# Kernel optimization log

Measured on AMD Instinct MI355X. Metric: run time of the kernel, lower is better.

## Reference

```python
import jax, jax.numpy as jnp
import numpy as np

N = 100000   # nodes
DEG = 4      # fixed out-degree (>2 so every node survives the c>2 mask)
E = N * DEG  # edges
IN = 128
H = 256


def _lin_params(key, fan_out, fan_in, bias=True):
    k1, k2 = jax.random.split(key)
    W = 0.05 * jax.random.normal(k1, (fan_out, fan_in), jnp.float32)
    if bias:
        b = 0.05 * jax.random.normal(k2, (fan_out,), jnp.float32)
        return W, b
    return W


def setup_inputs() -> dict:
    key = jax.random.key(0)
    ks = jax.random.split(key, 12)
    x = jax.random.normal(ks[0], (N, IN), jnp.float32)
    # every node has exactly DEG outgoing edges -> out-degree 4 > 2 for all nodes
    src = jnp.repeat(jnp.arange(N, dtype=jnp.int32), DEG)
    dst = jax.random.randint(ks[1], (E,), 0, N, dtype=jnp.int32)
    edge_index = jnp.stack([src, dst])  # [2, E]
    batch = jnp.zeros((N,), jnp.int32)
    Wr0, br0 = _lin_params(ks[2], H, IN)
    Ws0 = _lin_params(ks[3], H, IN, bias=False)
    Wr1, br1 = _lin_params(ks[4], H, H)
    Ws1 = _lin_params(ks[5], H, H, bias=False)
    Wr2, br2 = _lin_params(ks[6], H, H)
    Ws2 = _lin_params(ks[7], H, H, bias=False)
    Wsp1, bsp1 = _lin_params(ks[8], 1, H)
    Wsp2, bsp2 = _lin_params(ks[9], 1, H)
    Wl, bl = _lin_params(ks[10], 1, 2)
    return dict(x=x, edge_index=edge_index, batch=batch,
                Wr0=Wr0, br0=br0, Ws0=Ws0,
                Wr1=Wr1, br1=br1, Ws1=Ws1,
                Wr2=Wr2, br2=br2, Ws2=Ws2,
                Wsp1=Wsp1, bsp1=bsp1, Wsp2=Wsp2, bsp2=bsp2,
                Wl=Wl, bl=bl)


def reference(x, edge_index, batch, Wr0, br0, Ws0, Wr1, br1, Ws1,
              Wr2, br2, Ws2, Wsp1, bsp1, Wsp2, bsp2, Wl, bl):
    src, dst = edge_index[0], edge_index[1]

    def gconv(h, Wr, br, Ws):
        # PyG GraphConv(aggr='add'): out_i = W_rel @ sum_{j->i} h_j + b + W_root @ h_i
        agg = jax.ops.segment_sum(h[src], dst, num_segments=N)
        return jax.nn.relu(agg @ Wr.T + br + h @ Ws.T)

    h = gconv(x, Wr0, br0, Ws0)
    h = gconv(h, Wr1, br1, Ws1)
    h = gconv(h, Wr2, br2, Ws2)

    # unique(edge_index[0], counts) ; keep source nodes with out-degree > 2
    deg = jax.ops.segment_sum(jnp.ones((E,), h.dtype), src, num_segments=N)
    sel = jnp.nonzero(deg > 2, size=N, fill_value=0)[0]  # all N nodes by construction
    xs = h[sel].reshape(-1, 2 * H)  # pair consecutive nodes
    x1, x2 = xs[:, :H], xs[:, H:]
    out = jnp.concatenate([jax.nn.relu(x1 @ Wsp1.T + bsp1),
                           jax.nn.relu(x2 @ Wsp2.T + bsp2)], axis=1)
    y = jax.nn.sigmoid(out @ Wl.T + bl)  # split=True branch
    return y, xs, x1, x2
```

## Files before the change

kernel.cpp:

```cpp
#include <hip/hip_runtime.h>
#include <hip/hip_bf16.h>
#include <math.h>

#define NNODES 100000
#define NEDGES 400000
#define INDIM  128
#define HDIM   256
#define MAXDEG 32

#define BM 64
#define BN 256
#define BK 64
#define MTILES 1563

typedef __attribute__((ext_vector_type(8))) short short8;
typedef __attribute__((ext_vector_type(8))) unsigned short ushort8v;
typedef __attribute__((ext_vector_type(4))) float f32x4;

__device__ __forceinline__ float bf2f(unsigned short u) {
    union { unsigned int i; float f; } v; v.i = ((unsigned int)u) << 16; return v.f;
}
__device__ __forceinline__ unsigned short f2bf(float f) {
    union { float f; unsigned int i; } v; v.f = f;
    unsigned int r = v.i + 0x7fffu + ((v.i >> 16) & 1u);
    return (unsigned short)(r >> 16);
}

__device__ __forceinline__ void async_load16(const void* g, void* l) {
    __builtin_amdgcn_global_load_lds(
        (const __attribute__((address_space(1))) unsigned int*)g,
        (__attribute__((address_space(3))) unsigned int*)l,
        16, 0, 0);
}

#define XB_BLOCKS 12500
#define W0_BLOCKS 256
#define W1_BLOCKS 512
#define EL_BLOCKS 1563
#define PREP_BLOCKS (XB_BLOCKS + W0_BLOCKS + 2 * W1_BLOCKS + EL_BLOCKS)

__global__ void prep_kernel(const float* __restrict__ x, unsigned short* __restrict__ xb,
                            const float* __restrict__ Wr0, const float* __restrict__ Ws0,
                            unsigned short* __restrict__ B0,
                            const float* __restrict__ Wr1, const float* __restrict__ Ws1,
                            unsigned short* __restrict__ B1,
                            const float* __restrict__ Wr2, const float* __restrict__ Ws2,
                            unsigned short* __restrict__ B2,
                            const int* __restrict__ ei, int* __restrict__ cnt,
                            int* __restrict__ elist) {
    int b = blockIdx.x;
    if (b < XB_BLOCKS) {
        int i = b * 256 + threadIdx.x;
        float4 v = ((const float4*)x)[i];
        ushort4 o; o.x = f2bf(v.x); o.y = f2bf(v.y); o.z = f2bf(v.z); o.w = f2bf(v.w);
        ((ushort4*)xb)[i] = o;
        return;
    }
    b -= XB_BLOCKS;
    if (b < W0_BLOCKS + 2 * W1_BLOCKS) {
        const float *Wr, *Ws; unsigned short* B; int K;
        if (b < W0_BLOCKS)               { Wr = Wr0; Ws = Ws0; B = B0; K = INDIM; }
        else if (b < W0_BLOCKS + W1_BLOCKS) { Wr = Wr1; Ws = Ws1; B = B1; K = HDIM; b -= W0_BLOCKS; }
        else                              { Wr = Wr2; Ws = Ws2; B = B2; K = HDIM; b -= W0_BLOCKS + W1_BLOCKS; }
        int idx = b * 256 + threadIdx.x;
        int n = idx / (2 * K);
        int k = idx - n * 2 * K;
        float v = (k < K) ? Wr[n * K + k] : Ws[n * K + (k - K)];
        B[idx] = f2bf(v);
        return;
    }
    b -= W0_BLOCKS + 2 * W1_BLOCKS;
    int e = b * 256 + threadIdx.x;
    if (e < NEDGES) {
        int d = ei[NEDGES + e];
        int s = ei[e];
        int pos = atomicAdd(&cnt[d], 1);
        if (pos < MAXDEG) elist[d * MAXDEG + pos] = s;
    }
}

template<int MODE>
__global__ __launch_bounds__(256)
void fused_gconv(const unsigned short* __restrict__ h,
                 const int* __restrict__ cnt, const int* __restrict__ elist,
                 int K, const unsigned short* __restrict__ B, const float* __restrict__ bias,
                 unsigned short* __restrict__ hout,
                 float* __restrict__ xs, float* __restrict__ x1o, float* __restrict__ x2o,
                 const float* __restrict__ Wsp1, const float* __restrict__ Wsp2,
                 float* __restrict__ spart) {
    __shared__ __align__(16) unsigned char smem[65536];
    unsigned short* Agg = (unsigned short*)smem;
    unsigned short* Bsh = (unsigned short*)(smem + 32768);

    const int tid  = threadIdx.x;
    const int lane = tid & 63;
    const int wv   = tid >> 6;
    const int m0   = blockIdx.x * BM;
    const int Ktot = 2 * K;

    const int lane31 = lane & 31;
    const int hw     = lane >> 5;
    int pn = m0 + wv * 16 + (lane >> 2);
    if (pn >= NNODES) pn = NNODES - 1;
    const int4 elv = ((const int4*)(elist + (size_t)pn * MAXDEG))[lane & 3];
    int cnode = m0 + wv * 16 + (lane & 15);
    if (cnode >= NNODES) cnode = NNODES - 1;
    const int cv = cnt[cnode];

    #pragma unroll
    for (int it = 0; it < 8; it++) {
        int idx = it * 256 + tid;
        int row = idx >> 3, seg = idx & 7;
        int gseg = seg ^ (row & 7);
        async_load16(B + (size_t)row * Ktot + gseg * 8, &Bsh[idx * 8]);
    }

    if (K == 256) {
        for (int rd = 0; rd < 8; rd++) {
            const int iw = rd * 2 + hw;
            int cA = __shfl(cv, rd * 2);
            int cB = __shfl(cv, rd * 2 + 1);
            if (cA > MAXDEG) cA = MAXDEG;
            if (cB > MAXDEG) cB = MAXDEG;
            const int c    = hw ? cB : cA;
            const int cmax = cA > cB ? cA : cB;
            int node = m0 + wv * 16 + iw;
            if (node >= NNODES) node = NNODES - 1;
            float a[8];
            #pragma unroll
            for (int i = 0; i < 8; i++) a[i] = 0.f;
            for (int j0 = 0; j0 < cmax; j0 += 4) {
                int4 e;
                if (j0 < 16) {
                    int src = iw * 4 + (j0 >> 2);
                    e.x = __shfl(elv.x, src); e.y = __shfl(elv.y, src);
                    e.z = __shfl(elv.z, src); e.w = __shfl(elv.w, src);
                } else {
                    e = ((const int4*)(elist + (size_t)node * MAXDEG))[j0 >> 2];
                }
                int rem = c - j0;
                ushort8v v0 = {0,0,0,0,0,0,0,0}, v1 = v0, v2 = v0, v3 = v0;
                if (rem > 0) v0 = ((const ushort8v*)(h + (size_t)e.x * 256))[lane31];
                if (rem > 1) v1 = ((const ushort8v*)(h + (size_t)e.y * 256))[lane31];
                if (rem > 2) v2 = ((const ushort8v*)(h + (size_t)e.z * 256))[lane31];
                if (rem > 3) v3 = ((const ushort8v*)(h + (size_t)e.w * 256))[lane31];
                #pragma unroll
                for (int i = 0; i < 8; i++)
                    a[i] += bf2f(v0[i]) + bf2f(v1[i]) + bf2f(v2[i]) + bf2f(v3[i]);
            }
            int r = wv * 16 + iw;
            int sgp = (lane31 & ~7) | ((lane31 ^ r) & 7);
            ushort8v o;
            #pragma unroll
            for (int i = 0; i < 8; i++) o[i] = f2bf(a[i]);
            *(ushort8v*)&Agg[r * 256 + sgp * 8] = o;
        }
    } else {
        for (int rd = 0; rd < 8; rd++) {
            const int iw = rd * 2 + hw;
            int cA = __shfl(cv, rd * 2);
            int cB = __shfl(cv, rd * 2 + 1);
            if (cA > MAXDEG) cA = MAXDEG;
            if (cB > MAXDEG) cB = MAXDEG;
            const int c    = hw ? cB : cA;
            const int cmax = cA > cB ? cA : cB;
            int node = m0 + wv * 16 + iw;
            if (node >= NNODES) node = NNODES - 1;
            float a0 = 0.f, a1 = 0.f, a2 = 0.f, a3 = 0.f;
            for (int j0 = 0; j0 < cmax; j0 += 4) {
                int4 e;
                if (j0 < 16) {
                    int src = iw * 4 + (j0 >> 2);
                    e.x = __shfl(elv.x, src); e.y = __shfl(elv.y, src);
                    e.z = __shfl(elv.z, src); e.w = __shfl(elv.w, src);
                } else {
                    e = ((const int4*)(elist + (size_t)node * MAXDEG))[j0 >> 2];
                }
                int rem = c - j0;
                ushort4 v0 = {0,0,0,0}, v1 = {0,0,0,0}, v2 = {0,0,0,0}, v3 = {0,0,0,0};
                if (rem > 0) v0 = ((const ushort4*)(h + (size_t)e.x * 128))[lane31];
                if (rem > 1) v1 = ((const ushort4*)(h + (size_t)e.y * 128))[lane31];
                if (rem > 2) v2 = ((const ushort4*)(h + (size_t)e.z * 128))[lane31];
                if (rem > 3) v3 = ((const ushort4*)(h + (size_t)e.w * 128))[lane31];
                a0 += bf2f(v0.x) + bf2f(v1.x) + bf2f(v2.x) + bf2f(v3.x);
                a1 += bf2f(v0.y) + bf2f(v1.y) + bf2f(v2.y) + bf2f(v3.y);
                a2 += bf2f(v0.z) + bf2f(v1.z) + bf2f(v2.z) + bf2f(v3.z);
                a3 += bf2f(v0.w) + bf2f(v1.w) + bf2f(v2.w) + bf2f(v3.w);
            }
            int r = wv * 16 + iw;
            int sg = lane31 >> 1;
            int sgp = (sg & ~7) | ((sg ^ r) & 7);
            ushort4 o; o.x = f2bf(a0); o.y = f2bf(a1); o.z = f2bf(a2); o.w = f2bf(a3);
            *(ushort4*)&Agg[r * 128 + sgp * 8 + (lane31 & 1) * 4] = o;
        }
    }

    f32x4 acc[4][4];
    #pragma unroll
    for (int i = 0; i < 4; i++)
        #pragma unroll
        for (int j = 0; j < 4; j++)
            acc[i][j] = (f32x4){0.f, 0.f, 0.f, 0.f};

    for (int k0 = 0; k0 < Ktot; k0 += BK) {
        if (k0 >= K) {
            #pragma unroll
            for (int it = 0; it < 2; it++) {
                int idx = it * 256 + tid;
                int row = idx >> 3, seg = idx & 7;
                int gseg = seg ^ (row & 7);
                int grow = m0 + row; if (grow >= NNODES) grow = NNODES - 1;
                async_load16(h + (size_t)grow * K + (k0 - K) + gseg * 8, &Agg[idx * 8]);
            }
        }
        if (k0 > 0) {
            #pragma unroll
            for (int it = 0; it < 8; it++) {
                int idx = it * 256 + tid;
                int row = idx >> 3, seg = idx & 7;
                int gseg = seg ^ (row & 7);
                async_load16(B + (size_t)row * Ktot + k0 + gseg * 8, &Bsh[idx * 8]);
            }
        }
        __syncthreads();

        #pragma unroll
        for (int half = 0; half < 2; half++) {
            short8 af[4], bfr[4];
            if (k0 < K) {
                #pragma unroll
                for (int mt = 0; mt < 4; mt++) {
                    int ml = mt * 16 + (lane & 15);
                    int sg = (k0 >> 3) + half * 4 + (lane >> 4);
                    int sgp = (sg & ~7) | ((sg ^ ml) & 7);
                    af[mt] = *(const short8*)&Agg[ml * K + sgp * 8];
                }
            } else {
                #pragma unroll
                for (int mt = 0; mt < 4; mt++) {
                    int ml  = mt * 16 + (lane & 15);
                    int seg = half * 4 + (lane >> 4);
                    int ps  = seg ^ (ml & 7);
                    af[mt] = *(const short8*)&Agg[ml * BK + ps * 8];
                }
            }
            #pragma unroll
            for (int nt = 0; nt < 4; nt++) {
                int nl  = wv * 64 + nt * 16 + (lane & 15);
                int seg = half * 4 + (lane >> 4);
                int ps  = seg ^ (nl & 7);
                bfr[nt] = *(const short8*)&Bsh[nl * BK + ps * 8];
            }
            #pragma unroll
            for (int mt = 0; mt < 4; mt++)
                #pragma unroll
                for (int nt = 0; nt < 4; nt++)
                    acc[mt][nt] = __builtin_amdgcn_mfma_f32_16x16x32_bf16(
                        af[mt], bfr[nt], acc[mt][nt], 0, 0, 0);
        }
        __syncthreads();
    }

    float* bounce = (float*)smem;
    float* wb = bounce + wv * (16 * 68);
    const int q    = lane & 3;
    const int rrow = lane >> 2;

    #pragma unroll
    for (int mt = 0; mt < 4; mt++) {
        __syncthreads();
        #pragma unroll
        for (int nt = 0; nt < 4; nt++)
            #pragma unroll
            for (int rr = 0; rr < 4; rr++)
                wb[((lane >> 4) * 4 + rr) * 68 + nt * 16 + (lane & 15)] = acc[mt][nt][rr];
        __syncthreads();

        int grow = m0 + mt * 16 + rrow;
        int gc   = wv * 64 + q * 16;
        float4 v[4];
        #pragma unroll
        for (int s = 0; s < 4; s++)
            v[s] = ((const float4*)(wb + rrow * 68 + q * 16))[s];

        if (grow < NNODES) {
            const float4* bv = (const float4*)(bias + gc);
            #pragma unroll
            for (int s = 0; s < 4; s++) {
                float4 b4 = bv[s];
                v[s].x = fmaxf(v[s].x + b4.x, 0.f);
                v[s].y = fmaxf(v[s].y + b4.y, 0.f);
                v[s].z = fmaxf(v[s].z + b4.z, 0.f);
                v[s].w = fmaxf(v[s].w + b4.w, 0.f);
            }
            if (MODE == 0) {
                ushort8v o0, o1;
                o0[0]=f2bf(v[0].x); o0[1]=f2bf(v[0].y); o0[2]=f2bf(v[0].z); o0[3]=f2bf(v[0].w);
                o0[4]=f2bf(v[1].x); o0[5]=f2bf(v[1].y); o0[6]=f2bf(v[1].z); o0[7]=f2bf(v[1].w);
                o1[0]=f2bf(v[2].x); o1[1]=f2bf(v[2].y); o1[2]=f2bf(v[2].z); o1[3]=f2bf(v[2].w);
                o1[4]=f2bf(v[3].x); o1[5]=f2bf(v[3].y); o1[6]=f2bf(v[3].z); o1[7]=f2bf(v[3].w);
                ushort8v* dst = (ushort8v*)(hout + (size_t)grow * HDIM + gc);
                dst[0] = o0; dst[1] = o1;
            } else {
                float4* xsp = (float4*)(xs + (size_t)grow * HDIM + gc);
                #pragma unroll
                for (int s = 0; s < 4; s++) xsp[s] = v[s];
                float* xo = (grow & 1) ? x2o : x1o;
                float4* xop = (float4*)(xo + (size_t)(grow >> 1) * HDIM + gc);
                #pragma unroll
                for (int s = 0; s < 4; s++) xop[s] = v[s];
                const float* wsp = (grow & 1) ? Wsp2 : Wsp1;
                const float4* wv4 = (const float4*)(wsp + gc);
                float p = 0.f;
                #pragma unroll
                for (int s = 0; s < 4; s++) {
                    float4 w4 = wv4[s];
                    p += v[s].x * w4.x + v[s].y * w4.y + v[s].z * w4.z + v[s].w * w4.w;
                }
                p += __shfl_xor(p, 1);
                p += __shfl_xor(p, 2);
                if (q == 0) atomicAdd(&spart[grow], p);
            }
        }
    }
}

__global__ void finalize_kernel(const float* __restrict__ spart, const float* __restrict__ bsp1,
                                const float* __restrict__ bsp2, const float* __restrict__ Wl,
                                const float* __restrict__ bl, float* __restrict__ y) {
    int p = blockIdx.x * 256 + threadIdx.x;
    if (p < NNODES / 2) {
        float s1 = spart[2 * p]     + bsp1[0]; s1 = s1 > 0.f ? s1 : 0.f;
        float s2 = spart[2 * p + 1] + bsp2[0]; s2 = s2 > 0.f ? s2 : 0.f;
        float t = s1 * Wl[0] + s2 * Wl[1] + bl[0];
        y[p] = 1.f / (1.f + expf(-t));
    }
}

extern "C" void kernel_launch(void* const* d_in, const int* in_sizes, int n_in,
                              void* d_out, int out_size, void* d_ws, size_t ws_size,
                              hipStream_t stream) {
    const float* x    = (const float*)d_in[0];
    const int*   ei   = (const int*)d_in[1];
    const float* Wr0  = (const float*)d_in[3];
    const float* br0  = (const float*)d_in[4];
    const float* Ws0  = (const float*)d_in[5];
    const float* Wr1  = (const float*)d_in[6];
    const float* br1  = (const float*)d_in[7];
    const float* Ws1  = (const float*)d_in[8];
    const float* Wr2  = (const float*)d_in[9];
    const float* br2  = (const float*)d_in[10];
    const float* Ws2  = (const float*)d_in[11];
    const float* Wsp1 = (const float*)d_in[12];
    const float* bsp1 = (const float*)d_in[13];
    const float* Wsp2 = (const float*)d_in[14];
    const float* bsp2 = (const float*)d_in[15];
    const float* Wl   = (const float*)d_in[16];
    const float* bl   = (const float*)d_in[17];

    char* ws = (char*)d_ws;
    size_t off = 0;
    auto alloc = [&](size_t bytes) -> void* {
        void* p = ws + off;
        off += (bytes + 255) & ~(size_t)255;
        return p;
    };
    int*            cnt   = (int*)alloc((size_t)NNODES * 4);
    float*          spart = (float*)alloc((size_t)NNODES * 4);
    size_t zero_bytes = off;
    int*            elist = (int*)alloc((size_t)NNODES * MAXDEG * 4);
    unsigned short* xb    = (unsigned short*)alloc((size_t)NNODES * INDIM * 2);
    unsigned short* hA    = (unsigned short*)alloc((size_t)NNODES * HDIM * 2);
    unsigned short* hB    = (unsigned short*)alloc((size_t)NNODES * HDIM * 2);
    unsigned short* B0    = (unsigned short*)alloc((size_t)HDIM * 2 * INDIM * 2);
    unsigned short* B1    = (unsigned short*)alloc((size_t)HDIM * 2 * HDIM * 2);
    unsigned short* B2    = (unsigned short*)alloc((size_t)HDIM * 2 * HDIM * 2);

    float* y  = (float*)d_out;
    float* xs = y + 50000;
    float* x1 = xs + (size_t)50000 * 512;
    float* x2 = x1 + (size_t)50000 * 256;

    hipMemsetAsync(ws, 0, zero_bytes, stream);
    prep_kernel<<<PREP_BLOCKS, 256, 0, stream>>>(x, xb, Wr0, Ws0, B0, Wr1, Ws1, B1,
                                                 Wr2, Ws2, B2, ei, cnt, elist);

    fused_gconv<0><<<MTILES, 256, 0, stream>>>(xb, cnt, elist, INDIM, B0, br0, hA,
                                               nullptr, nullptr, nullptr,
                                               nullptr, nullptr, nullptr);
    fused_gconv<0><<<MTILES, 256, 0, stream>>>(hA, cnt, elist, HDIM, B1, br1, hB,
                                               nullptr, nullptr, nullptr,
                                               nullptr, nullptr, nullptr);
    fused_gconv<1><<<MTILES, 256, 0, stream>>>(hB, cnt, elist, HDIM, B2, br2, nullptr,
                                               xs, x1, x2, Wsp1, Wsp2, spart);
    finalize_kernel<<<(NNODES / 2 + 255) / 256, 256, 0, stream>>>(
        spart, bsp1, bsp2, Wl, bl, y);
}
```

Measured before the change: 603.7 us.

## Load GEMM operands directly from global, halve LDS, template K

Drops the LDS staging of the weight matrix B and of the root-feature tile. MFMA fragments are now read straight from global memory, and the root (h @ Ws) term is computed first so it can overlap the aggregation. LDS shrinks from 64KB to 32KB, K becomes a template parameter, and launch bounds request 3 blocks per CU to raise occupancy. The cost is uncoalesced, repeated global and L2 reads of B across waves with no LDS reuse, plus higher register pressure from fully unrolled loops.

```diff
diff --git a/kernel.cpp b/kernel.cpp
--- a/kernel.cpp
+++ b/kernel.cpp
@@ -24,13 +24,6 @@
     union { float f; unsigned int i; } v; v.f = f;
     unsigned int r = v.i + 0x7fffu + ((v.i >> 16) & 1u);
     return (unsigned short)(r >> 16);
-}
-
-__device__ __forceinline__ void async_load16(const void* g, void* l) {
-    __builtin_amdgcn_global_load_lds(
-        (const __attribute__((address_space(1))) unsigned int*)g,
-        (__attribute__((address_space(3))) unsigned int*)l,
-        16, 0, 0);
 }
 
 #define XB_BLOCKS 12500
@@ -79,24 +72,23 @@
     }
 }
 
-template<int MODE>
-__global__ __launch_bounds__(256)
+template<int MODE, int K>
+__global__ __launch_bounds__(256, 3)
 void fused_gconv(const unsigned short* __restrict__ h,
                  const int* __restrict__ cnt, const int* __restrict__ elist,
-                 int K, const unsigned short* __restrict__ B, const float* __restrict__ bias,
+                 const unsigned short* __restrict__ B, const float* __restrict__ bias,
                  unsigned short* __restrict__ hout,
                  float* __restrict__ xs, float* __restrict__ x1o, float* __restrict__ x2o,
                  const float* __restrict__ Wsp1, const float* __restrict__ Wsp2,
                  float* __restrict__ spart) {
-    __shared__ __align__(16) unsigned char smem[65536];
+    __shared__ __align__(16) unsigned char smem[32768];
     unsigned short* Agg = (unsigned short*)smem;
-    unsigned short* Bsh = (unsigned short*)(smem + 32768);
 
     const int tid  = threadIdx.x;
     const int lane = tid & 63;
     const int wv   = tid >> 6;
     const int m0   = blockIdx.x * BM;
-    const int Ktot = 2 * K;
+    constexpr int Ktot = 2 * K;
 
     const int lane31 = lane & 31;
     const int hw     = lane >> 5;
@@ -107,15 +99,7 @@
     if (cnode >= NNODES) cnode = NNODES - 1;
     const int cv = cnt[cnode];
 
-    #pragma unroll
-    for (int it = 0; it < 8; it++) {
-        int idx = it * 256 + tid;
-        int row = idx >> 3, seg = idx & 7;
-        int gseg = seg ^ (row & 7);
-        async_load16(B + (size_t)row * Ktot + gseg * 8, &Bsh[idx * 8]);
-    }
-
-    if (K == 256) {
+    if constexpr (K == 256) {
         for (int rd = 0; rd < 8; rd++) {
             const int iw = rd * 2 + hw;
             int cA = __shfl(cv, rd * 2);
@@ -202,54 +186,24 @@
         for (int j = 0; j < 4; j++)
             acc[i][j] = (f32x4){0.f, 0.f, 0.f, 0.f};
 
-    for (int k0 = 0; k0 < Ktot; k0 += BK) {
-        if (k0 >= K) {
-            #pragma unroll
-            for (int it = 0; it < 2; it++) {
-                int idx = it * 256 + tid;
-                int row = idx >> 3, seg = idx & 7;
-                int gseg = seg ^ (row & 7);
-                int grow = m0 + row; if (grow >= NNODES) grow = NNODES - 1;
-                async_load16(h + (size_t)grow * K + (k0 - K) + gseg * 8, &Agg[idx * 8]);
-            }
-        }
-        if (k0 > 0) {
-            #pragma unroll
-            for (int it = 0; it < 8; it++) {
-                int idx = it * 256 + tid;
-                int row = idx >> 3, seg = idx & 7;
-                int gseg = seg ^ (row & 7);
-                async_load16(B + (size_t)row * Ktot + k0 + gseg * 8, &Bsh[idx * 8]);
-            }
-        }
-        __syncthreads();
-
+    const int l15  = lane & 15;
+    const int seg0 = lane >> 4;
+
+    #pragma unroll
+    for (int k0 = 0; k0 < K; k0 += BK) {
         #pragma unroll
         for (int half = 0; half < 2; half++) {
+            const int seg = half * 4 + seg0;
             short8 af[4], bfr[4];
-            if (k0 < K) {
-                #pragma unroll
-                for (int mt = 0; mt < 4; mt++) {
-                    int ml = mt * 16 + (lane & 15);
-                    int sg = (k0 >> 3) + half * 4 + (lane >> 4);
-                    int sgp = (sg & ~7) | ((sg ^ ml) & 7);
-                    af[mt] = *(const short8*)&Agg[ml * K + sgp * 8];
-                }
-            } else {
-                #pragma unroll
-                for (int mt = 0; mt < 4; mt++) {
-                    int ml  = mt * 16 + (lane & 15);
-                    int seg = half * 4 + (lane >> 4);
-                    int ps  = seg ^ (ml & 7);
-                    af[mt] = *(const short8*)&Agg[ml * BK + ps * 8];
-                }
+            #pragma unroll
+            for (int mt = 0; mt < 4; mt++) {
+                int grow = m0 + mt * 16 + l15; if (grow >= NNODES) grow = NNODES - 1;
+                af[mt] = *(const short8*)(h + (size_t)grow * K + k0 + seg * 8);
             }
             #pragma unroll
             for (int nt = 0; nt < 4; nt++) {
-                int nl  = wv * 64 + nt * 16 + (lane & 15);
-                int seg = half * 4 + (lane >> 4);
-                int ps  = seg ^ (nl & 7);
-                bfr[nt] = *(const short8*)&Bsh[nl * BK + ps * 8];
+                int nl = wv * 64 + nt * 16 + l15;
+                bfr[nt] = *(const short8*)(B + (size_t)nl * Ktot + K + k0 + seg * 8);
             }
             #pragma unroll
             for (int mt = 0; mt < 4; mt++)
@@ -258,7 +212,35 @@
                     acc[mt][nt] = __builtin_amdgcn_mfma_f32_16x16x32_bf16(
                         af[mt], bfr[nt], acc[mt][nt], 0, 0, 0);
         }
-        __syncthreads();
+    }
+
+    __syncthreads();
+
+    #pragma unroll
+    for (int k0 = 0; k0 < K; k0 += BK) {
+        #pragma unroll
+        for (int half = 0; half < 2; half++) {
+            const int seg = half * 4 + seg0;
+            short8 af[4], bfr[4];
+            #pragma unroll
+            for (int nt = 0; nt < 4; nt++) {
+                int nl = wv * 64 + nt * 16 + l15;
+                bfr[nt] = *(const short8*)(B + (size_t)nl * Ktot + k0 + seg * 8);
+            }
+            #pragma unroll
+            for (int mt = 0; mt < 4; mt++) {
+                int ml = mt * 16 + l15;
+                int sg = (k0 >> 3) + seg;
+                int sgp = (sg & ~7) | ((sg ^ ml) & 7);
+                af[mt] = *(const short8*)&Agg[ml * K + sgp * 8];
+            }
+            #pragma unroll
+            for (int mt = 0; mt < 4; mt++)
+                #pragma unroll
+                for (int nt = 0; nt < 4; nt++)
+                    acc[mt][nt] = __builtin_amdgcn_mfma_f32_16x16x32_bf16(
+                        af[mt], bfr[nt], acc[mt][nt], 0, 0, 0);
+        }
     }
 
     float* bounce = (float*)smem;
@@ -385,14 +367,14 @@
     prep_kernel<<<PREP_BLOCKS, 256, 0, stream>>>(x, xb, Wr0, Ws0, B0, Wr1, Ws1, B1,
                                                  Wr2, Ws2, B2, ei, cnt, elist);
 
-    fused_gconv<0><<<MTILES, 256, 0, stream>>>(xb, cnt, elist, INDIM, B0, br0, hA,
-                                               nullptr, nullptr, nullptr,
-                                               nullptr, nullptr, nullptr);
-    fused_gconv<0><<<MTILES, 256, 0, stream>>>(hA, cnt, elist, HDIM, B1, br1, hB,
-                                               nullptr, nullptr, nullptr,
-                                               nullptr, nullptr, nullptr);
-    fused_gconv<1><<<MTILES, 256, 0, stream>>>(hB, cnt, elist, HDIM, B2, br2, nullptr,
-                                               xs, x1, x2, Wsp1, Wsp2, spart);
+    fused_gconv<0, 128><<<MTILES, 256, 0, stream>>>(xb, cnt, elist, B0, br0, hA,
+                                                    nullptr, nullptr, nullptr,
+                                                    nullptr, nullptr, nullptr);
+    fused_gconv<0, 256><<<MTILES, 256, 0, stream>>>(hA, cnt, elist, B1, br1, hB,
+                                                    nullptr, nullptr, nullptr,
+                                                    nullptr, nullptr, nullptr);
+    fused_gconv<1, 256><<<MTILES, 256, 0, stream>>>(hB, cnt, elist, B2, br2, nullptr,
+                                                    xs, x1, x2, Wsp1, Wsp2, spart);
     finalize_kernel<<<(NNODES / 2 + 255) / 256, 256, 0, stream>>>(
         spart, bsp1, bsp2, Wl, bl, y);
 }
```

After: 666.7 us. 10.4% more time.
